# Optimization experiments

Measured on AMD Instinct MI355X. Metric: run time of the kernel, lower is better.

Reference implementation:

```python
import jax, jax.numpy as jnp
import numpy as np

B, N, DIN, DOUT = 8, 2048, 256, 256

def setup_inputs() -> dict:
    key = jax.random.key(0)
    k1, k2, k3 = jax.random.split(key, 3)
    H = jax.random.normal(k1, (B, N, DIN), dtype=jnp.float32)
    G = jax.random.uniform(k2, (B, N, N), dtype=jnp.float32)  # positive -> nonzero row/col sums
    # xavier_uniform-style scale for the weight
    limit = float(np.sqrt(6.0 / (DIN + DOUT)))
    W = jax.random.uniform(k3, (DIN, DOUT), dtype=jnp.float32, minval=-limit, maxval=limit)
    return {"H": H, "G": G, "W": W}

def reference(H, G, W):
    # N_e = H @ W : [b,n,dout]
    N_e = H @ W
    # symmetric part
    G_F = (G + jnp.swapaxes(G, 1, 2)) * 0.5
    # loop over k of outer products == two normalized Gram matrices:
    # G_Sin[i,j] = sum_k G[k,i]*G[k,j] / rowsum_k  == G^T diag(1/rowsum) G
    # G_So[i,j]  = sum_k G[i,k]*G[j,k] / colsum_k  == G diag(1/colsum) G^T
    rs = G.sum(axis=-1)  # [b,n] row sums
    cs = G.sum(axis=-2)  # [b,n] col sums
    G_Sin = jnp.einsum('bki,bkj->bij', G / rs[:, :, None], G)
    G_So = jnp.einsum('bik,bjk->bij', G / cs[:, None, :], G)
    H_out = jnp.concatenate([
        jax.nn.relu(G_F @ N_e),
        jax.nn.relu(G_Sin @ N_e),
        jax.nn.relu(G_So @ N_e),
    ], axis=-1)  # [b,n,3*dout]
    return H_out
```

## Files before the change

### kernel.cpp

```cpp
#include <hip/hip_runtime.h>
#include <hip/hip_bf16.h>


constexpr int NN = 2048;
constexpr long GSTR = (long)NN * NN;

using frag8   = __attribute__((ext_vector_type(8))) short;
using floatx4 = __attribute__((ext_vector_type(4))) float;
using ush8    = __attribute__((ext_vector_type(8))) unsigned short;

__device__ inline unsigned short f2bf(float x) {
    unsigned u = __float_as_uint(x);
    u += 0x7FFF + ((u >> 16) & 1);
    return (unsigned short)(u >> 16);
}
__device__ inline float bf2f(unsigned short h) {
    return __uint_as_float((unsigned)h << 16);
}
__device__ inline ushort2 pk2(float a, float b) {
    union { __hip_bfloat162 h; ushort2 u; } cv;
    cv.h = __float22bfloat162_rn(float2{a, b});
    return cv.u;
}
__device__ inline void gload_lds16(const void* g, void* l) {
    __builtin_amdgcn_global_load_lds(
        (const __attribute__((address_space(1))) void*)g,
        (__attribute__((address_space(3))) void*)l, 16, 0, 0);
}

enum { EPI_NE = 0, EPI_M1 = 1, EPI_P2 = 2, EPI_O3 = 3 };
enum { A_F32ROW = 0, A_DMA = 1 };

template <int EPI, int AMODE, int TM>
__global__ __launch_bounds__(256) void mgemm(
    const void* __restrict__ Aptr,
    const unsigned short* __restrict__ B0,
    const unsigned short* __restrict__ B1,
    const float* __restrict__ rsraw,
    unsigned short* __restrict__ CsT,
    float* __restrict__ outp,
    const float* __restrict__ scale,
    int K, int lda, long strideA, long sB)
{
    constexpr int MF = TM / 32;
    __shared__ __align__(16) unsigned short As[TM * 64];
    __shared__ __align__(16) unsigned short Bs[64 * 64];

    const int t   = threadIdx.x;
    const int i0b = blockIdx.x * TM;
    const int j0  = blockIdx.y * 64;
    const int bb  = blockIdx.z;

    const unsigned short* Btb =
        ((EPI == EPI_P2 && j0 >= 256) ? B1 + (long)(j0 - 256) * K
                                      : B0 + (long)j0 * K) + (long)bb * sB;

    const int w = t >> 6, l = t & 63;
    const int wm = w >> 1, wn = w & 1;
    const int quad = l >> 4, c15 = l & 15;

    const int lr  = l >> 3, ls = l & 7;

    floatx4 acc[MF][2] = {};

    for (int k0 = 0; k0 < K; k0 += 64) {
        if constexpr (AMODE == A_DMA) {
            const unsigned short* Au = (const unsigned short*)Aptr + (long)bb * strideA;
            #pragma unroll
            for (int q = 0; q < TM / 32; ++q) {
                const int rt = q * 32 + w * 8;
                gload_lds16(Au + (long)(i0b + rt + lr) * lda + k0 + ((ls ^ lr) << 3),
                            &As[rt * 64]);
            }
        } else {
            const float* Af = (const float*)Aptr + (long)bb * strideA;
            const int ar  = t >> 2;
            const int ac0 = (t & 3) * 2;
            const float* ap = Af + (long)(i0b + ar) * lda + k0 + ac0 * 8;
            const float4 x0 = *(const float4*)(ap + 0);
            const float4 x1 = *(const float4*)(ap + 4);
            const float4 x2 = *(const float4*)(ap + 8);
            const float4 x3 = *(const float4*)(ap + 12);
            union { ush8 v; ushort2 u2[4]; } p0, p1;
            p0.u2[0] = pk2(x0.x, x0.y); p0.u2[1] = pk2(x0.z, x0.w);
            p0.u2[2] = pk2(x1.x, x1.y); p0.u2[3] = pk2(x1.z, x1.w);
            p1.u2[0] = pk2(x2.x, x2.y); p1.u2[1] = pk2(x2.z, x2.w);
            p1.u2[2] = pk2(x3.x, x3.y); p1.u2[3] = pk2(x3.z, x3.w);
            const int sw = ar & 7;
            *(ush8*)&As[ar * 64 + ((ac0 ^ sw) << 3)]       = p0.v;
            *(ush8*)&As[ar * 64 + (((ac0 + 1) ^ sw) << 3)] = p1.v;
        }
        #pragma unroll
        for (int q = 0; q < 2; ++q) {
            const int rt = w * 16 + q * 8;
            gload_lds16(Btb + (long)(rt + lr) * K + k0 + ((ls ^ lr) << 3),
                        &Bs[rt * 64]);
        }
        __syncthreads();

        #pragma unroll
        for (int ks = 0; ks < 2; ++ks) {
            frag8 af[MF], bfv[2];
            const int swr = c15 & 7;
            #pragma unroll
            for (int mt = 0; mt < MF; ++mt)
                af[mt] = *(const frag8*)&As[(wm * (TM / 2) + mt * 16 + c15) * 64
                                            + (((ks * 4 + quad) ^ swr) << 3)];
            #pragma unroll
            for (int nt = 0; nt < 2; ++nt)
                bfv[nt] = *(const frag8*)&Bs[(wn * 32 + nt * 16 + c15) * 64
                                             + (((ks * 4 + quad) ^ swr) << 3)];
            #pragma unroll
            for (int mt = 0; mt < MF; ++mt)
                #pragma unroll
                for (int nt = 0; nt < 2; ++nt)
                    acc[mt][nt] = __builtin_amdgcn_mfma_f32_16x16x32_bf16(
                        af[mt], bfv[nt], acc[mt][nt], 0, 0, 0);
        }
        __syncthreads();
    }

    const long rowb = (long)bb * NN;
    #pragma unroll
    for (int mt = 0; mt < MF; ++mt) {
        const int il = wm * (TM / 2) + mt * 16 + quad * 4;
        const int ib = i0b + il;
        float4 s4 = make_float4(1.f, 1.f, 1.f, 1.f);
        if constexpr (EPI == EPI_M1) s4 = *(const float4*)(scale + rowb + ib);
        if constexpr (EPI == EPI_P2) {
            if (j0 < 256) s4 = *(const float4*)(scale + rowb + ib);
        }
        #pragma unroll
        for (int nt = 0; nt < 2; ++nt) {
            floatx4 v = acc[mt][nt];
            const int gj = j0 + wn * 32 + nt * 16 + c15;
            if constexpr (EPI == EPI_NE) {
                union { ushort4 v; ushort2 u2[2]; } p;
                p.u2[0] = pk2(v[0], v[1]); p.u2[1] = pk2(v[2], v[3]);
                *(ushort4*)(CsT + ((long)bb * 256 + gj) * 2048 + ib) = p.v;
            } else if constexpr (EPI == EPI_M1) {
                union { ushort4 v; ushort2 u2[2]; } p;
                p.u2[0] = pk2(v[0] * s4.x, v[1] * s4.y);
                p.u2[1] = pk2(v[2] * s4.z, v[3] * s4.w);
                *(ushort4*)(CsT + ((long)bb * 256 + gj) * 2048 + ib) = p.v;
            } else if constexpr (EPI == EPI_P2) {
                if (j0 < 256) {
                    union { ushort4 v; ushort2 u2[2]; } p;
                    p.u2[0] = pk2(v[0] * s4.x, v[1] * s4.y);
                    p.u2[1] = pk2(v[2] * s4.z, v[3] * s4.w);
                    *(ushort4*)(CsT + ((long)bb * 256 + gj) * 2048 + ib) = p.v;
                    const float4 rr = *(const float4*)(rsraw + rowb + ib);
                    const ushort4 m1p = *(const ushort4*)(B1 + ((long)bb * 256 + gj) * 2048 + ib);
                    const float m1v[4] = {bf2f(m1p.x) * rr.x, bf2f(m1p.y) * rr.y,
                                          bf2f(m1p.z) * rr.z, bf2f(m1p.w) * rr.w};
                    #pragma unroll
                    for (int r = 0; r < 4; ++r)
                        outp[(rowb + ib + r) * 768 + gj] = fmaxf(0.5f * (v[r] + m1v[r]), 0.f);
                } else {
                    #pragma unroll
                    for (int r = 0; r < 4; ++r)
                        outp[(rowb + ib + r) * 768 + gj] = fmaxf(v[r], 0.f);
                }
            } else {
                #pragma unroll
                for (int r = 0; r < 4; ++r)
                    outp[(rowb + ib + r) * 768 + 512 + gj] = fmaxf(v[r], 0.f);
            }
        }
    }
}

__global__ __launch_bounds__(256) void cvt_g(
    const float* __restrict__ G,
    unsigned short* __restrict__ Gbf, unsigned short* __restrict__ GbfT,
    float* __restrict__ prs, float* __restrict__ pcs)
{
    __shared__ float Tf[64 * 65];
    __shared__ float cp[4][64];
    const int b = blockIdx.z;
    const int j0 = blockIdx.x * 64, i0 = blockIdx.y * 64;
    const int t = threadIdx.x;
    const int r = t >> 2, cb = (t & 3) * 16;

    float x[16];
    const long gbase = (long)b * GSTR + (long)(i0 + r) * NN + j0 + cb;
    #pragma unroll
    for (int q = 0; q < 4; ++q)
        *(float4*)&x[q * 4] = *(const float4*)(G + gbase + q * 4);

    union { ush8 v; ushort2 u2[4]; } pa, pb;
    #pragma unroll
    for (int q = 0; q < 4; ++q) pa.u2[q] = pk2(x[q * 2], x[q * 2 + 1]);
    #pragma unroll
    for (int q = 0; q < 4; ++q) pb.u2[q] = pk2(x[8 + q * 2], x[8 + q * 2 + 1]);
    *(ush8*)(Gbf + gbase)     = pa.v;
    *(ush8*)(Gbf + gbase + 8) = pb.v;

    float sr = 0.f;
    #pragma unroll
    for (int j = 0; j < 16; ++j) sr += x[j];
    sr += __shfl_xor(sr, 1);
    sr += __shfl_xor(sr, 2);
    if ((t & 3) == 0) prs[((long)b * 32 + blockIdx.x) * NN + i0 + r] = sr;

    #pragma unroll
    for (int j = 0; j < 16; ++j) Tf[r * 65 + cb + j] = x[j];
    __syncthreads();

    {
        const int col = t & 63, seg = t >> 6;
        float sc = 0.f;
        #pragma unroll
        for (int rr = 0; rr < 16; ++rr) sc += Tf[(seg * 16 + rr) * 65 + col];
        cp[seg][col] = sc;
    }
    __syncthreads();
    if (t < 64)
        pcs[((long)b * 32 + blockIdx.y) * NN + j0 + t] =
            cp[0][t] + cp[1][t] + cp[2][t] + cp[3][t];

    const int co = t >> 2, rb = (t & 3) * 16;
    unsigned short* dst = GbfT + (long)b * GSTR + (long)(j0 + co) * NN + i0 + rb;
    union { ush8 v; ushort2 u2[4]; } qa, qb;
    #pragma unroll
    for (int q = 0; q < 4; ++q)
        qa.u2[q] = pk2(Tf[(rb + q * 2) * 65 + co], Tf[(rb + q * 2 + 1) * 65 + co]);
    #pragma unroll
    for (int q = 0; q < 4; ++q)
        qb.u2[q] = pk2(Tf[(rb + 8 + q * 2) * 65 + co], Tf[(rb + 8 + q * 2 + 1) * 65 + co]);
    *(ush8*)(dst)     = qa.v;
    *(ush8*)(dst + 8) = qb.v;
}

__global__ __launch_bounds__(256) void finalize(
    const float* __restrict__ prs, const float* __restrict__ pcs,
    float* __restrict__ inv_rs, float* __restrict__ rs_raw,
    float* __restrict__ inv_cs,
    const float* __restrict__ W, unsigned short* __restrict__ Wt)
{
    const int idx = blockIdx.x * 256 + threadIdx.x;
    if (blockIdx.y == 0) {
        const int b = idx >> 11, i = idx & 2047;
        float s = 0.f;
        #pragma unroll
        for (int jc = 0; jc < 32; ++jc) s += prs[((long)b * 32 + jc) * NN + i];
        inv_rs[idx] = 1.0f / s;
        rs_raw[idx] = s;
    } else if (blockIdx.y == 1) {
        const int b = idx >> 11, i = idx & 2047;
        float s = 0.f;
        #pragma unroll
        for (int jc = 0; jc < 32; ++jc) s += pcs[((long)b * 32 + jc) * NN + i];
        inv_cs[idx] = 1.0f / s;
    } else {
        #pragma unroll
        for (int e = 0; e < 4; ++e) {
            const int flat = idx * 4 + e;
            const int j = flat >> 8, k = flat & 255;
            Wt[flat] = f2bf(W[(long)k * 256 + j]);
        }
    }
}

extern "C" void kernel_launch(void* const* d_in, const int* in_sizes, int n_in,
                              void* d_out, int out_size, void* d_ws, size_t ws_size,
                              hipStream_t stream)
{
    constexpr int B = 8;
    const float* H = (const float*)d_in[0];
    const float* G = (const float*)d_in[1];
    const float* W = (const float*)d_in[2];
    float* out = (float*)d_out;

    unsigned short* ws16 = (unsigned short*)d_ws;
    unsigned short* Gbf  = ws16;
    unsigned short* GbfT = Gbf  + (long)B * GSTR;
    unsigned short* Wt   = GbfT + (long)B * GSTR;
    unsigned short* NeT  = Wt   + 65536;
    unsigned short* M1sT = NeT  + 4194304;
    unsigned short* M2sT = M1sT + 4194304;
    float* inv_rs = (float*)(M2sT + 4194304);
    float* rs_raw = inv_rs + 16384;
    float* inv_cs = rs_raw + 16384;
    float* prs    = inv_cs + 16384;
    float* pcs    = prs + (long)B * 32 * NN;

    cvt_g<<<dim3(32, 32, 8), 256, 0, stream>>>(G, Gbf, GbfT, prs, pcs);
    finalize<<<dim3(64, 3), 256, 0, stream>>>(prs, pcs, inv_rs, rs_raw, inv_cs, W, Wt);

    const long sNT = 256L * NN;
    mgemm<EPI_NE, A_F32ROW, 64><<<dim3(32, 4, 8), 256, 0, stream>>>(
        H, Wt, nullptr, nullptr, NeT, nullptr, nullptr,
        256, 256, 2048L * 256, 0);
    mgemm<EPI_M1, A_DMA, 128><<<dim3(16, 4, 8), 256, 0, stream>>>(
        Gbf, NeT, nullptr, nullptr, M1sT, nullptr, inv_rs,
        2048, 2048, GSTR, sNT);
    mgemm<EPI_P2, A_DMA, 128><<<dim3(16, 8, 8), 256, 0, stream>>>(
        GbfT, NeT, M1sT, rs_raw, M2sT, out, inv_cs,
        2048, 2048, GSTR, sNT);
    mgemm<EPI_O3, A_DMA, 128><<<dim3(16, 4, 8), 256, 0, stream>>>(
        Gbf, M2sT, nullptr, nullptr, nullptr, out, nullptr,
        2048, 2048, GSTR, sNT);
}
```

Measured before the change: 390.7 us.

## Rewrite G conversion kernel with 128x128 tiles and bf16 swizzled LDS transpose

The fp32-to-bf16 conversion/transpose kernel now processes 128x128 tiles. Each thread reads full 32-byte row segments, and the transpose is staged in LDS as bf16 with an XOR-style rotated layout instead of padded fp32. Column sums are accumulated in registers and reduced with shuffles rather than a second LDS pass. Partial row/column sums shrink from 32 to 16 chunks, and finalize is updated to match. The aim is better coalescing, half the LDS traffic and fewer blocks for this bandwidth-bound pass, at the cost of more registers per thread and fewer blocks for latency hiding.

```diff
diff --git a/kernel.cpp b/kernel.cpp
--- a/kernel.cpp
+++ b/kernel.cpp
@@ -175,61 +175,68 @@
     unsigned short* __restrict__ Gbf, unsigned short* __restrict__ GbfT,
     float* __restrict__ prs, float* __restrict__ pcs)
 {
-    __shared__ float Tf[64 * 65];
-    __shared__ float cp[4][64];
-    const int b = blockIdx.z;
-    const int j0 = blockIdx.x * 64, i0 = blockIdx.y * 64;
-    const int t = threadIdx.x;
-    const int r = t >> 2, cb = (t & 3) * 16;
-
-    float x[16];
-    const long gbase = (long)b * GSTR + (long)(i0 + r) * NN + j0 + cb;
+    __shared__ __align__(16) unsigned short Tb[128 * 136];
+    __shared__ float cpw[4][128];
+
+    const int b  = blockIdx.z;
+    const int j0 = blockIdx.x * 128, i0 = blockIdx.y * 128;
+    const int t  = threadIdx.x;
+    const int c  = t & 15;
+    const int rg = t >> 4;
+    const int w  = t >> 6, l16 = (t & 63) >> 4;
+
+    float cs[8] = {};
+
     #pragma unroll
-    for (int q = 0; q < 4; ++q)
-        *(float4*)&x[q * 4] = *(const float4*)(G + gbase + q * 4);
-
-    union { ush8 v; ushort2 u2[4]; } pa, pb;
+    for (int p = 0; p < 8; ++p) {
+        const int row = p * 16 + rg;
+        const long gb = (long)b * GSTR + (long)(i0 + row) * NN + j0 + c * 8;
+        const float4 x0 = *(const float4*)(G + gb);
+        const float4 x1 = *(const float4*)(G + gb + 4);
+        union { ush8 v; ushort2 u2[4]; } pk;
+        pk.u2[0] = pk2(x0.x, x0.y); pk.u2[1] = pk2(x0.z, x0.w);
+        pk.u2[2] = pk2(x1.x, x1.y); pk.u2[3] = pk2(x1.z, x1.w);
+        *(ush8*)(Gbf + gb) = pk.v;
+        *(ush8*)&Tb[row * 136 + (((c + (row >> 3)) & 15) << 3)] = pk.v;
+
+        float rp = x0.x + x0.y + x0.z + x0.w + x1.x + x1.y + x1.z + x1.w;
+        rp += __shfl_xor(rp, 1);
+        rp += __shfl_xor(rp, 2);
+        rp += __shfl_xor(rp, 4);
+        rp += __shfl_xor(rp, 8);
+        if (c == 0) prs[((long)b * 16 + blockIdx.x) * NN + i0 + row] = rp;
+
+        cs[0] += x0.x; cs[1] += x0.y; cs[2] += x0.z; cs[3] += x0.w;
+        cs[4] += x1.x; cs[5] += x1.y; cs[6] += x1.z; cs[7] += x1.w;
+    }
+
     #pragma unroll
-    for (int q = 0; q < 4; ++q) pa.u2[q] = pk2(x[q * 2], x[q * 2 + 1]);
+    for (int e = 0; e < 8; ++e) {
+        cs[e] += __shfl_xor(cs[e], 16);
+        cs[e] += __shfl_xor(cs[e], 32);
+    }
+    if (l16 == 0) {
+        #pragma unroll
+        for (int e = 0; e < 8; ++e) cpw[w][c * 8 + e] = cs[e];
+    }
+    __syncthreads();
+    if (t < 128)
+        pcs[((long)b * 16 + blockIdx.y) * NN + j0 + t] =
+            cpw[0][t] + cpw[1][t] + cpw[2][t] + cpw[3][t];
+
     #pragma unroll
-    for (int q = 0; q < 4; ++q) pb.u2[q] = pk2(x[8 + q * 2], x[8 + q * 2 + 1]);
-    *(ush8*)(Gbf + gbase)     = pa.v;
-    *(ush8*)(Gbf + gbase + 8) = pb.v;
-
-    float sr = 0.f;
-    #pragma unroll
-    for (int j = 0; j < 16; ++j) sr += x[j];
-    sr += __shfl_xor(sr, 1);
-    sr += __shfl_xor(sr, 2);
-    if ((t & 3) == 0) prs[((long)b * 32 + blockIdx.x) * NN + i0 + r] = sr;
-
-    #pragma unroll
-    for (int j = 0; j < 16; ++j) Tf[r * 65 + cb + j] = x[j];
-    __syncthreads();
-
-    {
-        const int col = t & 63, seg = t >> 6;
-        float sc = 0.f;
-        #pragma unroll
-        for (int rr = 0; rr < 16; ++rr) sc += Tf[(seg * 16 + rr) * 65 + col];
-        cp[seg][col] = sc;
-    }
-    __syncthreads();
-    if (t < 64)
-        pcs[((long)b * 32 + blockIdx.y) * NN + j0 + t] =
-            cp[0][t] + cp[1][t] + cp[2][t] + cp[3][t];
-
-    const int co = t >> 2, rb = (t & 3) * 16;
-    unsigned short* dst = GbfT + (long)b * GSTR + (long)(j0 + co) * NN + i0 + rb;
-    union { ush8 v; ushort2 u2[4]; } qa, qb;
-    #pragma unroll
-    for (int q = 0; q < 4; ++q)
-        qa.u2[q] = pk2(Tf[(rb + q * 2) * 65 + co], Tf[(rb + q * 2 + 1) * 65 + co]);
-    #pragma unroll
-    for (int q = 0; q < 4; ++q)
-        qb.u2[q] = pk2(Tf[(rb + 8 + q * 2) * 65 + co], Tf[(rb + 8 + q * 2 + 1) * 65 + co]);
-    *(ush8*)(dst)     = qa.v;
-    *(ush8*)(dst + 8) = qb.v;
+    for (int q = 0; q < 8; ++q) {
+        const int jr = q * 16 + rg;
+        const int sbase = ((jr >> 3) << 3);
+        union { ush8 v; unsigned short a[8]; } pk;
+        #pragma unroll
+        for (int r = 0; r < 8; ++r) {
+            const int i = c * 8 + r;
+            pk.a[r] = Tb[i * 136 + ((((jr >> 3) + c) & 15) << 3) + (jr & 7)];
+        }
+        (void)sbase;
+        *(ush8*)(GbfT + (long)b * GSTR + (long)(j0 + jr) * NN + i0 + c * 8) = pk.v;
+    }
 }
 
 __global__ __launch_bounds__(256) void finalize(
@@ -243,14 +250,14 @@
         const int b = idx >> 11, i = idx & 2047;
         float s = 0.f;
         #pragma unroll
-        for (int jc = 0; jc < 32; ++jc) s += prs[((long)b * 32 + jc) * NN + i];
+        for (int jc = 0; jc < 16; ++jc) s += prs[((long)b * 16 + jc) * NN + i];
         inv_rs[idx] = 1.0f / s;
         rs_raw[idx] = s;
     } else if (blockIdx.y == 1) {
         const int b = idx >> 11, i = idx & 2047;
         float s = 0.f;
         #pragma unroll
-        for (int jc = 0; jc < 32; ++jc) s += pcs[((long)b * 32 + jc) * NN + i];
+        for (int ic = 0; ic < 16; ++ic) s += pcs[((long)b * 16 + ic) * NN + i];
         inv_cs[idx] = 1.0f / s;
     } else {
         #pragma unroll
@@ -283,9 +290,9 @@
     float* rs_raw = inv_rs + 16384;
     float* inv_cs = rs_raw + 16384;
     float* prs    = inv_cs + 16384;
-    float* pcs    = prs + (long)B * 32 * NN;
-
-    cvt_g<<<dim3(32, 32, 8), 256, 0, stream>>>(G, Gbf, GbfT, prs, pcs);
+    float* pcs    = prs + (long)B * 16 * NN;
+
+    cvt_g<<<dim3(16, 16, 8), 256, 0, stream>>>(G, Gbf, GbfT, prs, pcs);
     finalize<<<dim3(64, 3), 256, 0, stream>>>(prs, pcs, inv_rs, rs_raw, inv_cs, W, Wt);
 
     const long sNT = 256L * NN;
```

Result: no change. 383.4 us (-1.9%).
